# Kernel optimization log

Hardware: AMD Instinct MI355X
Metric: run time of the kernel (lower is better)

Reference implementation:

```python
import jax, jax.numpy as jnp
import numpy as np
from math import sqrt


def setup_inputs() -> dict:
    key = jax.random.key(0)
    kq, kk, kv = jax.random.split(key, 3)
    B, L, S, H, E, D = 2, 4096, 4096, 8, 64, 64
    queries = jax.random.normal(kq, (B, L, H, E), dtype=jnp.float32)
    keys = jax.random.normal(kk, (B, S, H, E), dtype=jnp.float32)
    values = jax.random.normal(kv, (B, S, H, D), dtype=jnp.float32)
    attn_mask = jnp.zeros((1,), dtype=bool)  # unused (mask_flag=False)
    return {"queries": queries, "keys": keys, "values": values, "attn_mask": attn_mask}


def reference(queries, keys, values, attn_mask):
    # queries: [B,L,H,E], keys: [B,S,H,E], values: [B,S,H,D]
    E = queries.shape[-1]
    scale = 1.0 / sqrt(E)
    # log-domain value preprocessing: exp(V - max_over_seq(V))
    value_max = jnp.max(values, axis=1, keepdims=True)  # [B,1,H,D]
    v_exp = jnp.exp(values - value_max)                 # [B,S,H,D]
    # standard QK^T softmax (mask_flag=False, dropout=0 in eval)
    scores = jnp.einsum('blhe,bshe->bhls', queries, keys)  # [B,H,L,S]
    A = jax.nn.softmax(scale * scores, axis=-1)
    V = jnp.einsum('bhls,bshd->blhd', A, v_exp)            # [B,L,H,D]
    # log-domain postprocessing: log(AV) + value_max (broadcasts over L)
    V = jnp.log(V) + value_max
    return V
```

## Files before the change

### kernel.cpp

```cpp
#include <hip/hip_runtime.h>
#include <math.h>

#define NB 2
#define NL 4096
#define NS 4096
#define NH 8
#define NE 64
#define ND 64
#define SB 64
#define NT (NS / SB)
#define GT (NT / 2)
#define TILE_B 8192
#define LOG2E 1.4426950408889634f
#define SC2 (0.125f * LOG2E)

typedef __attribute__((ext_vector_type(8))) short bf16x8;
typedef __attribute__((ext_vector_type(4))) float f32x4;
typedef __attribute__((ext_vector_type(16))) float f32x16;
typedef unsigned short ushort_t;

__device__ __forceinline__ short f2bf(float f) {
  union { float f; unsigned u; } v; v.f = f;
  unsigned u = v.u;
  return (short)((u + 0x7fffu + ((u >> 16) & 1u)) >> 16);
}

__device__ __forceinline__ unsigned cvt_pk_bf16(float lo, float hi) {
  unsigned r;
  asm("v_cvt_pk_bf16_f32 %0, %1, %2" : "=v"(r) : "v"(lo), "v"(hi));
  return r;
}

__device__ __forceinline__ void gload16(const void* g, void* l) {
  __builtin_amdgcn_global_load_lds(
      (const __attribute__((address_space(1))) void*)g,
      (__attribute__((address_space(3))) void*)l, 16, 0, 0);
}


__global__ __launch_bounds__(256) void kvprep(const float* __restrict__ Kg,
                                              const float* __restrict__ Vg,
                                              ushort_t* __restrict__ kimg,
                                              ushort_t* __restrict__ vimg) {
  int blk = blockIdx.x;
  int bh = blk >> 6, tile = blk & 63;
  int b = bh >> 3, h = bh & 7;
  int t = threadIdx.x;
  int srow = t >> 2, c16 = (t & 3) * 16;
  {
    const float4* p4 =
        (const float4*)(Kg + (((size_t)b * NS + tile * SB + srow) * NH + h) * NE + c16);
    float4 a = p4[0], bq = p4[1], c = p4[2], d = p4[3];
    unsigned u0 = cvt_pk_bf16(a.x, a.y), u1 = cvt_pk_bf16(a.z, a.w);
    unsigned u2 = cvt_pk_bf16(bq.x, bq.y), u3 = cvt_pk_bf16(bq.z, bq.w);
    unsigned u4 = cvt_pk_bf16(c.x, c.y), u5 = cvt_pk_bf16(c.z, c.w);
    unsigned u6 = cvt_pk_bf16(d.x, d.y), u7 = cvt_pk_bf16(d.z, d.w);
    char* base = (char*)kimg + (size_t)blk * TILE_B;
    int off0 = (c16 >> 4) * 2048 + (srow >> 5) * 1024 + (srow & 31) * 16;
    uint4 w0 = {u0, u1, u2, u3}, w1 = {u4, u5, u6, u7};
    *(uint4*)(base + off0) = w0;
    *(uint4*)(base + off0 + 512) = w1;
  }
  {
    __shared__ short Vsh[64 * 72];
    const float4* p4 =
        (const float4*)(Vg + (((size_t)b * NS + tile * SB + srow) * NH + h) * ND + c16);
    float4 va = p4[0], vb = p4[1], vc = p4[2], vd = p4[3];
    float fv[16] = {va.x, va.y, va.z, va.w, vb.x, vb.y, vb.z, vb.w,
                    vc.x, vc.y, vc.z, vc.w, vd.x, vd.y, vd.z, vd.w};
#pragma unroll
    for (int i = 0; i < 16; ++i)
      Vsh[(c16 + i) * 72 + srow] = f2bf(__expf(fv[i]));
    __syncthreads();
    int dr = t >> 2, sc = (t & 3) * 16;
    bf16x8 o0 = *(const bf16x8*)&Vsh[dr * 72 + sc];
    bf16x8 o1 = *(const bf16x8*)&Vsh[dr * 72 + sc + 8];
    char* base = (char*)vimg + (size_t)blk * TILE_B;
    int off0 = (sc >> 4) * 2048 + (dr >> 5) * 1024 + (dr & 31) * 16;
    *(bf16x8*)(base + off0) = o0;
    *(bf16x8*)(base + off0 + 512) = o1;
  }
}

__global__ __launch_bounds__(512) void laser_fast(
    const float* __restrict__ Qg, const ushort_t* __restrict__ Kimg,
    const ushort_t* __restrict__ Vimg, float* __restrict__ Og) {
  int orig = blockIdx.x;
  int bid = (orig & 7) * 64 + (orig >> 3);
  int qt = bid & 31;
  int bh = bid >> 5;
  int b = bh >> 3, hh = bh & 7;
  int t = threadIdx.x;
  int w = t >> 6;
  int grp = w >> 2;
  int wi = w & 3;
  int lane = t & 63;
  int lq = lane & 31;
  int h = lane >> 5;

  __shared__ __attribute__((aligned(16))) char smem[34816];
  char* kls = smem + grp * 16384;

  const char* kbase = (const char*)Kimg + (size_t)bh * (NT * TILE_B);
  const char* vbase = (const char*)Vimg + (size_t)bh * (NT * TILE_B);

  int q0 = qt * 128 + wi * 32;
  const float* qp = Qg + (((size_t)b * NL + q0 + lq) * NH + hh) * NE;
  bf16x8 qf[4];
#pragma unroll
  for (int kk = 0; kk < 4; ++kk) {
    int e0 = 16 * kk + 8 * h;
    float4 x = *(const float4*)(qp + e0);
    float4 y = *(const float4*)(qp + e0 + 4);
    union { bf16x8 v; unsigned u[4]; } tm;
    tm.u[0] = cvt_pk_bf16(x.x * SC2, x.y * SC2);
    tm.u[1] = cvt_pk_bf16(x.z * SC2, x.w * SC2);
    tm.u[2] = cvt_pk_bf16(y.x * SC2, y.y * SC2);
    tm.u[3] = cvt_pk_bf16(y.z * SC2, y.w * SC2);
    qf[kk] = tm.v;
  }

  f32x16 acc0, acc1;
  float l_r = 0.f;
#pragma unroll
  for (int i = 0; i < 16; ++i) { acc0[i] = 0.f; acc1[i] = 0.f; }

  int soff = wi * 2048 + lane * 16;
  int tbase = grp * GT;
  int fb = h * 512 + lq * 16;

#define STAGE_K(buf, ti)                                                     \
  do {                                                                       \
    const char* ks = kbase + (size_t)(tbase + (ti)) * TILE_B + soff;         \
    gload16(ks, kls + (buf) * 8192 + wi * 2048);                             \
    gload16(ks + 1024, kls + (buf) * 8192 + wi * 2048 + 1024);               \
  } while (0)

#define MAKE_PA(P, g, idx)                                                   \
    do {                                                                     \
      unsigned a0 = cvt_pk_bf16(P[8 * (g) + 0], P[8 * (g) + 1]);             \
      unsigned a1 = cvt_pk_bf16(P[8 * (g) + 2], P[8 * (g) + 3]);             \
      unsigned b0 = cvt_pk_bf16(P[8 * (g) + 4], P[8 * (g) + 5]);             \
      unsigned b1 = cvt_pk_bf16(P[8 * (g) + 6], P[8 * (g) + 7]);             \
      auto w02 = __builtin_amdgcn_permlane32_swap(a0, b0, false, false);     \
      auto w13 = __builtin_amdgcn_permlane32_swap(a1, b1, false, false);     \
      union { bf16x8 v; unsigned u[4]; } tm;                                 \
      tm.u[0] = w02[0]; tm.u[1] = w13[0]; tm.u[2] = w02[1]; tm.u[3] = w13[1];\
      pa[idx] = tm.v;                                                        \
    } while (0)

  STAGE_K(0, 0);
  asm volatile("s_waitcnt vmcnt(0)" ::: "memory");
  __syncthreads();
  int cur = 0;

  for (int ti = 0; ti < GT; ++ti) {
    if (ti + 1 < GT) STAGE_K(cur ^ 1, ti + 1);

    const char* Kc = kls + cur * 8192;

    f32x16 s0, s1;
#pragma unroll
    for (int i = 0; i < 16; ++i) { s0[i] = 0.f; s1[i] = 0.f; }
    __builtin_amdgcn_s_setprio(1);
#pragma unroll
    for (int kk = 0; kk < 4; ++kk) {
      bf16x8 ka = *(const bf16x8*)(Kc + fb + kk * 2048);
      bf16x8 kb = *(const bf16x8*)(Kc + fb + kk * 2048 + 1024);
      s0 = __builtin_amdgcn_mfma_f32_32x32x16_bf16(ka, qf[kk], s0, 0, 0, 0);
      s1 = __builtin_amdgcn_mfma_f32_32x32x16_bf16(kb, qf[kk], s1, 0, 0, 0);
    }
    __builtin_amdgcn_s_setprio(0);

#pragma unroll
    for (int i = 0; i < 16; ++i) {
      s0[i] = __builtin_amdgcn_exp2f(s0[i]);
      s1[i] = __builtin_amdgcn_exp2f(s1[i]);
    }
    {
      float t0 = (s0[0] + s0[1]) + (s0[2] + s0[3]);
      float t1 = (s0[4] + s0[5]) + (s0[6] + s0[7]);
      float t2 = (s0[8] + s0[9]) + (s0[10] + s0[11]);
      float t3 = (s0[12] + s0[13]) + (s0[14] + s0[15]);
      float t4 = (s1[0] + s1[1]) + (s1[2] + s1[3]);
      float t5 = (s1[4] + s1[5]) + (s1[6] + s1[7]);
      float t6 = (s1[8] + s1[9]) + (s1[10] + s1[11]);
      float t7 = (s1[12] + s1[13]) + (s1[14] + s1[15]);
      l_r += ((t0 + t1) + (t2 + t3)) + ((t4 + t5) + (t6 + t7));
    }

    bf16x8 pa[4];
    MAKE_PA(s0, 0, 0);
    MAKE_PA(s0, 1, 1);
    MAKE_PA(s1, 0, 2);
    MAKE_PA(s1, 1, 3);

    const char* vtile = vbase + (size_t)(tbase + ti) * TILE_B + fb;
    __builtin_amdgcn_s_setprio(1);
#pragma unroll
    for (int kk = 0; kk < 4; ++kk) {
      bf16x8 v0 = *(const bf16x8*)(vtile + kk * 2048);
      bf16x8 v1 = *(const bf16x8*)(vtile + kk * 2048 + 1024);
      acc0 = __builtin_amdgcn_mfma_f32_32x32x16_bf16(pa[kk], v0, acc0, 0, 0, 0);
      acc1 = __builtin_amdgcn_mfma_f32_32x32x16_bf16(pa[kk], v1, acc1, 0, 0, 0);
    }
    __builtin_amdgcn_s_setprio(0);

    asm volatile("s_waitcnt vmcnt(0)" ::: "memory");
    __syncthreads();
    cur ^= 1;
  }
#undef STAGE_K
#undef MAKE_PA

  float* exch = (float*)(void*)smem;
  float* lex  = (float*)(void*)(smem + 32768);
  float* lsm  = (float*)(void*)(smem + 33792);
  if (grp == 1) {
    float* e = exch + wi * 2048 + lane;
#pragma unroll
    for (int r = 0; r < 16; ++r) {
      e[r * 64] = acc0[r];
      e[(16 + r) * 64] = acc1[r];
    }
    lex[wi * 64 + lane] = l_r;
  }
  __syncthreads();
  if (grp == 0) {
    float* e = exch + wi * 2048 + lane;
#pragma unroll
    for (int r = 0; r < 16; ++r) {
      acc0[r] += e[r * 64];
      acc1[r] += e[(16 + r) * 64];
    }
    l_r += lex[wi * 64 + lane];

    union { float f; unsigned u; } cu;
    cu.f = l_r;
    auto mm = __builtin_amdgcn_permlane32_swap(cu.u, cu.u, false, false);
    union { unsigned u; float f; } m0, m1;
    m0.u = mm[0]; m1.u = mm[1];
    lsm[wi * 32 + lq] = m0.f + m1.f;

#pragma unroll
    for (int r = 0; r < 16; ++r) {
      int q = (r & 3) + 8 * (r >> 2) + 4 * h;
      float logl = __logf(lsm[wi * 32 + q]);
      size_t o = (((size_t)b * NL + q0 + q) * NH + hh) * ND + lq;
      Og[o] = __logf(acc0[r]) - logl;
      Og[o + 32] = __logf(acc1[r]) - logl;
    }
  }
}

__global__ void vmax_partial(const float* __restrict__ Vp, float* __restrict__ part) {
  int blk = blockIdx.x;
  int bh = blk >> 4, ck = blk & 15;
  int b = bh >> 3, h = bh & 7;
  int t = threadIdx.x;
  int d = t & 63, g = t >> 6;
  const float* base = Vp + (((size_t)b * NS + ck * 256) * NH + h) * ND + d;
  float m = -INFINITY;
  for (int s = g; s < 256; s += 4)
    m = fmaxf(m, base[(size_t)s * NH * ND]);
  __shared__ float red[4][64];
  red[g][d] = m;
  __syncthreads();
  if (t < 64)
    part[(size_t)blk * 64 + t] =
        fmaxf(fmaxf(red[0][t], red[1][t]), fmaxf(red[2][t], red[3][t]));
}

__global__ void vmax_reduce(const float* __restrict__ part, float* __restrict__ vmax) {
  int bh = blockIdx.x, t = threadIdx.x;
  float m = -INFINITY;
#pragma unroll
  for (int c = 0; c < 16; ++c)
    m = fmaxf(m, part[((size_t)bh * 16 + c) * 64 + t]);
  vmax[bh * 64 + t] = m;
}

__global__ __launch_bounds__(256) void laser_slow(
    const float* __restrict__ Qg, const float* __restrict__ Kg,
    const float* __restrict__ Vg, const float* __restrict__ vmax,
    float* __restrict__ Og) {
  int bid = blockIdx.x;
  int qt = bid & 63;
  int bh = bid >> 6;
  int b = bh >> 3, h = bh & 7;
  int t = threadIdx.x;
  int w = t >> 6;
  int lane = t & 63;
  int lr = lane & 15;
  int lg = lane >> 4;

  __shared__ short Kt[SB * NE];
  __shared__ short Vt[ND * SB];
  __shared__ short Pl[4][16 * SB];
  __shared__ float vmx[ND];

  if (t < ND) vmx[t] = vmax[bh * ND + t];

  int q0 = qt * 64;
  int qrow = q0 + w * 16 + lr;
  const float* qptr = Qg + (((size_t)b * NL + qrow) * NH + h) * NE;
  bf16x8 qf[2];
#pragma unroll
  for (int kf = 0; kf < 2; ++kf) {
    const float4* p4 = (const float4*)(qptr + kf * 32 + lg * 8);
    float4 a = p4[0], bq = p4[1];
    qf[kf][0] = f2bf(a.x);  qf[kf][1] = f2bf(a.y);
    qf[kf][2] = f2bf(a.z);  qf[kf][3] = f2bf(a.w);
    qf[kf][4] = f2bf(bq.x); qf[kf][5] = f2bf(bq.y);
    qf[kf][6] = f2bf(bq.z); qf[kf][7] = f2bf(bq.w);
  }

  f32x4 acc_o[4];
  float m_r[4], l_r[4];
  const f32x4 fzero = {0.f, 0.f, 0.f, 0.f};
#pragma unroll
  for (int i = 0; i < 4; ++i) { acc_o[i] = fzero; m_r[i] = -INFINITY; l_r[i] = 0.f; }

  const float scale = 0.125f;
  int srow = t >> 2;
  int c16 = (t & 3) * 16;

  for (int s0 = 0; s0 < NS; s0 += SB) {
    __syncthreads();
    {
      const float4* kp4 =
          (const float4*)(Kg + (((size_t)b * NS + (s0 + srow)) * NH + h) * NE + c16);
      float4 t0 = kp4[0], t1 = kp4[1], t2 = kp4[2], t3 = kp4[3];
      bf16x8 c0, c1;
      c0[0] = f2bf(t0.x); c0[1] = f2bf(t0.y); c0[2] = f2bf(t0.z); c0[3] = f2bf(t0.w);
      c0[4] = f2bf(t1.x); c0[5] = f2bf(t1.y); c0[6] = f2bf(t1.z); c0[7] = f2bf(t1.w);
      c1[0] = f2bf(t2.x); c1[1] = f2bf(t2.y); c1[2] = f2bf(t2.z); c1[3] = f2bf(t2.w);
      c1[4] = f2bf(t3.x); c1[5] = f2bf(t3.y); c1[6] = f2bf(t3.z); c1[7] = f2bf(t3.w);
      int base = srow * 128 + c16 * 2;
      int swz = (srow & 7) << 4;
      *(bf16x8*)((char*)Kt + ((base) ^ swz)) = c0;
      *(bf16x8*)((char*)Kt + ((base + 16) ^ swz)) = c1;
    }
    {
      const float4* vp4 =
          (const float4*)(Vg + (((size_t)b * NS + (s0 + srow)) * NH + h) * ND + c16);
      float4 t0 = vp4[0], t1 = vp4[1], t2 = vp4[2], t3 = vp4[3];
      float fv[16] = {t0.x, t0.y, t0.z, t0.w, t1.x, t1.y, t1.z, t1.w,
                      t2.x, t2.y, t2.z, t2.w, t3.x, t3.y, t3.z, t3.w};
#pragma unroll
      for (int i = 0; i < 16; ++i) {
        int d = c16 + i;
        int byte = (d * 128 + srow * 2) ^ ((d & 7) << 4);
        *(short*)((char*)Vt + byte) = f2bf(__expf(fv[i] - vmx[d]));
      }
    }
    __syncthreads();

    f32x4 sacc[4];
#pragma unroll
    for (int jt = 0; jt < 4; ++jt) sacc[jt] = fzero;
#pragma unroll
    for (int jt = 0; jt < 4; ++jt) {
      int srw = jt * 16 + lr;
      int rb = srw * 128;
      int swz = (srw & 7) << 4;
      bf16x8 kb0 = *(const bf16x8*)((const char*)Kt + ((rb + lg * 16) ^ swz));
      bf16x8 kb1 = *(const bf16x8*)((const char*)Kt + ((rb + 64 + lg * 16) ^ swz));
      sacc[jt] = __builtin_amdgcn_mfma_f32_16x16x32_bf16(qf[0], kb0, sacc[jt], 0, 0, 0);
      sacc[jt] = __builtin_amdgcn_mfma_f32_16x16x32_bf16(qf[1], kb1, sacc[jt], 0, 0, 0);
    }

    float mnew[4], corr[4];
#pragma unroll
    for (int r = 0; r < 4; ++r) {
      float x = fmaxf(fmaxf(sacc[0][r], sacc[1][r]),
                      fmaxf(sacc[2][r], sacc[3][r])) * scale;
      x = fmaxf(x, __shfl_xor(x, 1));
      x = fmaxf(x, __shfl_xor(x, 2));
      x = fmaxf(x, __shfl_xor(x, 4));
      x = fmaxf(x, __shfl_xor(x, 8));
      mnew[r] = fmaxf(m_r[r], x);
      corr[r] = __expf(m_r[r] - mnew[r]);
    }
    float rs[4] = {0.f, 0.f, 0.f, 0.f};
    short pb[4][4];
#pragma unroll
    for (int jt = 0; jt < 4; ++jt)
#pragma unroll
      for (int r = 0; r < 4; ++r) {
        float p = __expf(sacc[jt][r] * scale - mnew[r]);
        rs[r] += p;
        pb[jt][r] = f2bf(p);
      }
#pragma unroll
    for (int r = 0; r < 4; ++r) {
      float x = rs[r];
      x += __shfl_xor(x, 1);
      x += __shfl_xor(x, 2);
      x += __shfl_xor(x, 4);
      x += __shfl_xor(x, 8);
      l_r[r] = l_r[r] * corr[r] + x;
      m_r[r] = mnew[r];
    }
    short* pwv = &Pl[w][0];
#pragma unroll
    for (int jt = 0; jt < 4; ++jt)
#pragma unroll
      for (int r = 0; r < 4; ++r) {
        int row = lg * 4 + r, col = jt * 16 + lr;
        int byte = (row * 128 + col * 2) ^ ((row & 7) << 4);
        *(short*)((char*)pwv + byte) = pb[jt][r];
      }
#pragma unroll
    for (int dt = 0; dt < 4; ++dt)
#pragma unroll
      for (int r = 0; r < 4; ++r) acc_o[dt][r] *= corr[r];
#pragma unroll
    for (int kf = 0; kf < 2; ++kf) {
      int ab = lr * 128;
      int aswz = (lr & 7) << 4;
      bf16x8 pa = *(const bf16x8*)((const char*)pwv + ((ab + kf * 64 + lg * 16) ^ aswz));
#pragma unroll
      for (int dt = 0; dt < 4; ++dt) {
        int drow = dt * 16 + lr;
        int vb_byte = (drow * 128 + kf * 64 + lg * 16) ^ ((drow & 7) << 4);
        bf16x8 vb = *(const bf16x8*)((const char*)Vt + vb_byte);
        acc_o[dt] = __builtin_amdgcn_mfma_f32_16x16x32_bf16(pa, vb, acc_o[dt], 0, 0, 0);
      }
    }
  }

#pragma unroll
  for (int r = 0; r < 4; ++r) {
    int row = q0 + w * 16 + lg * 4 + r;
    float logl = __logf(l_r[r]);
#pragma unroll
    for (int dt = 0; dt < 4; ++dt) {
      int d = dt * 16 + lr;
      Og[(((size_t)b * NL + row) * NH + h) * ND + d] =
          __logf(acc_o[dt][r]) - logl + vmx[d];
    }
  }
}

extern "C" void kernel_launch(void* const* d_in, const int* in_sizes, int n_in,
                              void* d_out, int out_size, void* d_ws, size_t ws_size,
                              hipStream_t stream) {
  (void)in_sizes; (void)n_in; (void)out_size;
  const float* Q = (const float*)d_in[0];
  const float* K = (const float*)d_in[1];
  const float* V = (const float*)d_in[2];
  float* out = (float*)d_out;

  float* vmax = (float*)d_ws;
  float* part = (float*)((char*)d_ws + 4096);
  const size_t kimg_off = 1u << 20;
  const size_t vimg_off = (size_t)9u << 20;
  const size_t img_bytes = (size_t)16 * NT * TILE_B;
  bool fast = ws_size >= vimg_off + img_bytes;

  if (fast) {
    ushort_t* kimg = (ushort_t*)((char*)d_ws + kimg_off);
    ushort_t* vimg = (ushort_t*)((char*)d_ws + vimg_off);
    kvprep<<<dim3(1024), dim3(256), 0, stream>>>(K, V, kimg, vimg);
    laser_fast<<<dim3(512), dim3(512), 0, stream>>>(Q, kimg, vimg, out);
  } else {
    vmax_partial<<<dim3(256), dim3(256), 0, stream>>>(V, part);
    vmax_reduce<<<dim3(16), dim3(64), 0, stream>>>(part, vmax);
    laser_slow<<<dim3(1024), dim3(256), 0, stream>>>(Q, K, V, vmax, out);
  }
}
```

Measured before the change: 97.71 us.

## Split KV sequence four ways per 32-query block, load K directly from global

Each block now handles 32 queries with 4 waves, and each wave processes a quarter of the key sequence. Partial accumulators are combined through a two-level tree reduction in LDS. The K staging through LDS via global_load_lds and its per-tile barriers is removed, so K fragments are read straight from global memory as V already was. This aims to remove per-iteration synchronization and raise parallelism (2048 smaller blocks), but it gives up K tile sharing across the four query waves, increasing global/L2 traffic for K.

Result: slower. 134.6 us (+37.8%).

```diff
diff --git a/kernel.cpp b/kernel.cpp
--- a/kernel.cpp
+++ b/kernel.cpp
@@ -9,7 +9,7 @@
 #define ND 64
 #define SB 64
 #define NT (NS / SB)
-#define GT (NT / 2)
+#define GT4 (NT / 4)
 #define TILE_B 8192
 #define LOG2E 1.4426950408889634f
 #define SC2 (0.125f * LOG2E)
@@ -29,12 +29,6 @@
   unsigned r;
   asm("v_cvt_pk_bf16_f32 %0, %1, %2" : "=v"(r) : "v"(lo), "v"(hi));
   return r;
-}
-
-__device__ __forceinline__ void gload16(const void* g, void* l) {
-  __builtin_amdgcn_global_load_lds(
-      (const __attribute__((address_space(1))) void*)g,
-      (__attribute__((address_space(3))) void*)l, 16, 0, 0);
 }
 
 
@@ -82,29 +76,29 @@
   }
 }
 
-__global__ __launch_bounds__(512) void laser_fast(
+__global__ __launch_bounds__(256) void laser_fast(
     const float* __restrict__ Qg, const ushort_t* __restrict__ Kimg,
     const ushort_t* __restrict__ Vimg, float* __restrict__ Og) {
   int orig = blockIdx.x;
-  int bid = (orig & 7) * 64 + (orig >> 3);
-  int qt = bid & 31;
-  int bh = bid >> 5;
+  int bid = (orig & 7) * 256 + (orig >> 3);
+  int qt = bid & 127;
+  int bh = bid >> 7;
   int b = bh >> 3, hh = bh & 7;
   int t = threadIdx.x;
-  int w = t >> 6;
-  int grp = w >> 2;
-  int wi = w & 3;
+  int grp = t >> 6;
   int lane = t & 63;
   int lq = lane & 31;
   int h = lane >> 5;
 
-  __shared__ __attribute__((aligned(16))) char smem[34816];
-  char* kls = smem + grp * 16384;
-
-  const char* kbase = (const char*)Kimg + (size_t)bh * (NT * TILE_B);
-  const char* vbase = (const char*)Vimg + (size_t)bh * (NT * TILE_B);
-
-  int q0 = qt * 128 + wi * 32;
+  __shared__ __attribute__((aligned(16))) char smem[17024];
+
+  int fb = h * 512 + lq * 16;
+  const char* kbase = (const char*)Kimg + (size_t)bh * (NT * TILE_B) +
+                      (size_t)grp * (GT4 * TILE_B) + fb;
+  const char* vbase = (const char*)Vimg + (size_t)bh * (NT * TILE_B) +
+                      (size_t)grp * (GT4 * TILE_B) + fb;
+
+  int q0 = qt * 32;
   const float* qp = Qg + (((size_t)b * NL + q0 + lq) * NH + hh) * NE;
   bf16x8 qf[4];
 #pragma unroll
@@ -124,17 +118,6 @@
   float l_r = 0.f;
 #pragma unroll
   for (int i = 0; i < 16; ++i) { acc0[i] = 0.f; acc1[i] = 0.f; }
-
-  int soff = wi * 2048 + lane * 16;
-  int tbase = grp * GT;
-  int fb = h * 512 + lq * 16;
-
-#define STAGE_K(buf, ti)                                                     \
-  do {                                                                       \
-    const char* ks = kbase + (size_t)(tbase + (ti)) * TILE_B + soff;         \
-    gload16(ks, kls + (buf) * 8192 + wi * 2048);                             \
-    gload16(ks + 1024, kls + (buf) * 8192 + wi * 2048 + 1024);               \
-  } while (0)
 
 #define MAKE_PA(P, g, idx)                                                   \
     do {                                                                     \
@@ -149,15 +132,10 @@
       pa[idx] = tm.v;                                                        \
     } while (0)
 
-  STAGE_K(0, 0);
-  asm volatile("s_waitcnt vmcnt(0)" ::: "memory");
-  __syncthreads();
-  int cur = 0;
-
-  for (int ti = 0; ti < GT; ++ti) {
-    if (ti + 1 < GT) STAGE_K(cur ^ 1, ti + 1);
-
-    const char* Kc = kls + cur * 8192;
+#pragma unroll 1
+  for (int ti = 0; ti < GT4; ++ti) {
+    const char* kt = kbase + (size_t)ti * TILE_B;
+    const char* vt = vbase + (size_t)ti * TILE_B;
 
     f32x16 s0, s1;
 #pragma unroll
@@ -165,8 +143,8 @@
     __builtin_amdgcn_s_setprio(1);
 #pragma unroll
     for (int kk = 0; kk < 4; ++kk) {
-      bf16x8 ka = *(const bf16x8*)(Kc + fb + kk * 2048);
-      bf16x8 kb = *(const bf16x8*)(Kc + fb + kk * 2048 + 1024);
+      bf16x8 ka = *(const bf16x8*)(kt + kk * 2048);
+      bf16x8 kb = *(const bf16x8*)(kt + kk * 2048 + 1024);
       s0 = __builtin_amdgcn_mfma_f32_32x32x16_bf16(ka, qf[kk], s0, 0, 0, 0);
       s1 = __builtin_amdgcn_mfma_f32_32x32x16_bf16(kb, qf[kk], s1, 0, 0, 0);
     }
@@ -195,57 +173,71 @@
     MAKE_PA(s1, 0, 2);
     MAKE_PA(s1, 1, 3);
 
-    const char* vtile = vbase + (size_t)(tbase + ti) * TILE_B + fb;
     __builtin_amdgcn_s_setprio(1);
 #pragma unroll
     for (int kk = 0; kk < 4; ++kk) {
-      bf16x8 v0 = *(const bf16x8*)(vtile + kk * 2048);
-      bf16x8 v1 = *(const bf16x8*)(vtile + kk * 2048 + 1024);
+      bf16x8 v0 = *(const bf16x8*)(vt + kk * 2048);
+      bf16x8 v1 = *(const bf16x8*)(vt + kk * 2048 + 1024);
       acc0 = __builtin_amdgcn_mfma_f32_32x32x16_bf16(pa[kk], v0, acc0, 0, 0, 0);
       acc1 = __builtin_amdgcn_mfma_f32_32x32x16_bf16(pa[kk], v1, acc1, 0, 0, 0);
     }
     __builtin_amdgcn_s_setprio(0);
-
-    asm volatile("s_waitcnt vmcnt(0)" ::: "memory");
-    __syncthreads();
-    cur ^= 1;
-  }
-#undef STAGE_K
+  }
 #undef MAKE_PA
 
   float* exch = (float*)(void*)smem;
-  float* lex  = (float*)(void*)(smem + 32768);
-  float* lsm  = (float*)(void*)(smem + 33792);
-  if (grp == 1) {
-    float* e = exch + wi * 2048 + lane;
+  float* lex  = (float*)(void*)(smem + 16384);
+  float* lsm  = (float*)(void*)(smem + 16896);
+  if (grp & 1) {
+    float* e = exch + (grp >> 1) * 2048 + lane;
 #pragma unroll
     for (int r = 0; r < 16; ++r) {
       e[r * 64] = acc0[r];
       e[(16 + r) * 64] = acc1[r];
     }
-    lex[wi * 64 + lane] = l_r;
+    lex[(grp >> 1) * 64 + lane] = l_r;
   }
   __syncthreads();
-  if (grp == 0) {
-    float* e = exch + wi * 2048 + lane;
+  if (!(grp & 1)) {
+    float* e = exch + (grp >> 1) * 2048 + lane;
 #pragma unroll
     for (int r = 0; r < 16; ++r) {
       acc0[r] += e[r * 64];
       acc1[r] += e[(16 + r) * 64];
     }
-    l_r += lex[wi * 64 + lane];
+    l_r += lex[(grp >> 1) * 64 + lane];
+  }
+  __syncthreads();
+  if (grp == 2) {
+    float* e = exch + lane;
+#pragma unroll
+    for (int r = 0; r < 16; ++r) {
+      e[r * 64] = acc0[r];
+      e[(16 + r) * 64] = acc1[r];
+    }
+    lex[lane] = l_r;
+  }
+  __syncthreads();
+  if (grp == 0) {
+    float* e = exch + lane;
+#pragma unroll
+    for (int r = 0; r < 16; ++r) {
+      acc0[r] += e[r * 64];
+      acc1[r] += e[(16 + r) * 64];
+    }
+    l_r += lex[lane];
 
     union { float f; unsigned u; } cu;
     cu.f = l_r;
     auto mm = __builtin_amdgcn_permlane32_swap(cu.u, cu.u, false, false);
     union { unsigned u; float f; } m0, m1;
     m0.u = mm[0]; m1.u = mm[1];
-    lsm[wi * 32 + lq] = m0.f + m1.f;
+    lsm[lq] = m0.f + m1.f;
 
 #pragma unroll
     for (int r = 0; r < 16; ++r) {
       int q = (r & 3) + 8 * (r >> 2) + 4 * h;
-      float logl = __logf(lsm[wi * 32 + q]);
+      float logl = __logf(lsm[q]);
       size_t o = (((size_t)b * NL + q0 + q) * NH + hh) * ND + lq;
       Og[o] = __logf(acc0[r]) - logl;
       Og[o + 32] = __logf(acc1[r]) - logl;
@@ -463,7 +455,7 @@
     ushort_t* kimg = (ushort_t*)((char*)d_ws + kimg_off);
     ushort_t* vimg = (ushort_t*)((char*)d_ws + vimg_off);
     kvprep<<<dim3(1024), dim3(256), 0, stream>>>(K, V, kimg, vimg);
-    laser_fast<<<dim3(512), dim3(512), 0, stream>>>(Q, kimg, vimg, out);
+    laser_fast<<<dim3(2048), dim3(256), 0, stream>>>(Q, kimg, vimg, out);
   } else {
     vmax_partial<<<dim3(256), dim3(256), 0, stream>>>(V, part);
     vmax_reduce<<<dim3(16), dim3(64), 0, stream>>>(part, vmax);
```
